# Performance work log

Hardware: AMD Instinct MI355X
Metric: run time of the kernel (lower is better)

Reference implementation:

```python
import jax, jax.numpy as jnp
import numpy as np

B, T, F, H = 4096, 48, 64, 128


def _uniform(key, shape, stdv):
    return jax.random.uniform(key, shape, jnp.float32, -stdv, stdv)


def setup_inputs() -> dict:
    key = jax.random.key(0)
    ks = jax.random.split(key, 24)
    values = jax.random.normal(ks[0], (B, T, F), jnp.float32)
    masks = (jax.random.uniform(ks[1], (B, T, F)) < 0.8).astype(jnp.float32)
    deltas = jax.random.uniform(ks[2], (B, T, F), jnp.float32)
    sH = 1.0 / np.sqrt(H)
    sF = 1.0 / np.sqrt(F)
    inp = {
        "values": values, "masks": masks, "deltas": deltas,
        # TemporalDecay h: W [H, F], b [H] (stdv = 1/sqrt(out=H))
        "Wdh": _uniform(ks[3], (H, F), sH), "bdh": _uniform(ks[4], (H,), sH),
        # TemporalDecay x (diag): W [F, F], b [F]
        "Wdx": _uniform(ks[5], (F, F), sF), "bdx": _uniform(ks[6], (F,), sF),
        # hist_reg: Linear(H -> F)
        "Wh": _uniform(ks[7], (F, H), sH), "bh": _uniform(ks[8], (F,), sH),
        # feat_reg: masked F x F
        "Wf": _uniform(ks[9], (F, F), sF), "bf": _uniform(ks[10], (F,), sF),
        # weight_combine: Linear(2F -> F)
        "Wc": _uniform(ks[11], (F, 2 * F), 1.0 / np.sqrt(2 * F)),
        "bc": _uniform(ks[12], (F,), 1.0 / np.sqrt(2 * F)),
        # LSTMCell(2F -> H): gates in PyTorch order i, f, g, o
        "W_ih": _uniform(ks[13], (4 * H, 2 * F), sH),
        "W_hh": _uniform(ks[14], (4 * H, H), sH),
        "b_ih": _uniform(ks[15], (4 * H,), sH),
        "b_hh": _uniform(ks[16], (4 * H,), sH),
        # out: Linear(H -> 1)
        "Wo": _uniform(ks[17], (1, H), sH), "bo": _uniform(ks[18], (1,), sH),
    }
    return inp


def reference(values, masks, deltas, Wdh, bdh, Wdx, bdx, Wh, bh, Wf, bf,
              Wc, bc, W_ih, W_hh, b_ih, b_hh, Wo, bo):
    impute_weight = 1.0
    b, t, f = values.shape
    h_dim = Wdh.shape[0]
    eye = jnp.eye(f, dtype=values.dtype)
    Wdx_m = Wdx * eye            # diagonal temporal decay
    Wf_m = Wf * (1.0 - eye)

    def step(carry, xt):
        h, c, loss = carry
        x, m, d = xt  # each [B, F]
        gamma_h = jnp.exp(-jax.nn.relu(d @ Wdh.T + bdh))        # [B, H]
        gamma_x = jnp.exp(-jax.nn.relu(d @ Wdx_m.T + bdx))      # [B, F]
        h = h * gamma_h
        x_h = h @ Wh.T + bh
        denom = jnp.sum(m) + 1e-5
        loss = loss + jnp.sum(jnp.abs(x - x_h) * m) / denom
        x_c = m * x + (1.0 - m) * x_h
        z_h = x_c @ Wf_m.T + bf
        loss = loss + jnp.sum(jnp.abs(x - z_h) * m) / denom
        alpha = jnp.concatenate([gamma_x, m], axis=1) @ Wc.T + bc
        c_h = alpha * z_h + (1.0 - alpha) * x_h
        loss = loss + jnp.sum(jnp.abs(x - c_h) * m) / denom
        c_c = m * x + (1.0 - m) * c_h
        inputs = jnp.concatenate([c_c, m], axis=1)  # [B, 2F]
        gates = inputs @ W_ih.T + b_ih + h @ W_hh.T + b_hh
        i_g, f_g, g_g, o_g = jnp.split(gates, 4, axis=1)
        c = jax.nn.sigmoid(f_g) * c + jax.nn.sigmoid(i_g) * jnp.tanh(g_g)
        h = jax.nn.sigmoid(o_g) * jnp.tanh(c)
        return (h, c, loss), c_c

    init = (jnp.zeros((b, h_dim), values.dtype),
            jnp.zeros((b, h_dim), values.dtype),
            jnp.zeros((), values.dtype))
    xs = (jnp.swapaxes(values, 0, 1),
          jnp.swapaxes(masks, 0, 1),
          jnp.swapaxes(deltas, 0, 1))
    (h, c, x_loss), imps = jax.lax.scan(step, init, xs)
    imputations = jnp.swapaxes(imps, 0, 1)  # [B, T, F]
    predictions = h @ Wo.T + bo             # [B, 1]
    return x_loss * impute_weight, imputations, predictions
```

## Files before the change

kernel.cpp:

```cpp
#include <hip/hip_runtime.h>
#include <hip/hip_bf16.h>
#include <math.h>

#define BB 4096
#define TT 48
#define FF 64
#define HH 128
#define ROWS 16
#define NT 512
#define NBLK (BB / ROWS)

typedef __attribute__((ext_vector_type(8))) short short8;
typedef __attribute__((ext_vector_type(4))) float f32x4;

#define MFMA(a, b, c) __builtin_amdgcn_mfma_f32_16x16x32_bf16((a), (b), (c), 0, 0, 0)

__device__ __forceinline__ float sigm(float x) { return 1.f / (1.f + __expf(-x)); }
__device__ __forceinline__ float tanh_f(float x) { return 2.f / (1.f + __expf(-2.f * x)) - 1.f; }

__global__ __launch_bounds__(256) void prep_kernel(
    const float* __restrict__ W_ih, const float* __restrict__ W_hh,
    const float* __restrict__ Wdh,  const float* __restrict__ Wh,
    const float* __restrict__ Wf,   const float* __restrict__ Wc,
    __hip_bfloat16* __restrict__ frags) {
    const int idx = blockIdx.x * 256 + threadIdx.x;
    float v;
    if (idx < 131072) {
        const int jj = idx & 7;
        const int lane = (idx >> 3) & 63;
        const int ks = (idx >> 9) & 7;
        const int tile = idx >> 12;
        const int n = tile * 16 + (lane & 15);
        const int k = ks * 32 + ((lane >> 4) << 3) + jj;
        v = (k < 128) ? W_ih[n * 128 + k] : W_hh[n * 128 + (k - 128)];
    } else {
        const int u = idx - 131072;
        const int jj = u & 7;
        const int lane = (u >> 3) & 63;
        const int lq = lane & 15, q8 = (lane >> 4) << 3;
        if (u < 8192) {
            const int ks = (u >> 9) & 1, nt = u >> 10;
            const int n = nt * 16 + lq, k = ks * 32 + q8 + jj;
            v = Wdh[n * 64 + k];
        } else if (u < 16384) {
            const int uu = u - 8192;
            const int ks = (uu >> 9) & 3, nt = uu >> 11;
            const int n = nt * 16 + lq, k = ks * 32 + q8 + jj;
            v = Wh[n * 128 + k];
        } else if (u < 20480) {
            const int uu = u - 16384;
            const int ks = (uu >> 9) & 1, nt = uu >> 10;
            const int n = nt * 16 + lq, k = ks * 32 + q8 + jj;
            v = (k == n) ? 0.f : Wf[n * 64 + k];
        } else {
            const int uu = u - 20480;
            const int ks = (uu >> 9) & 3, nt = uu >> 11;
            const int n = nt * 16 + lq, k = ks * 32 + q8 + jj;
            v = Wc[n * 128 + k];
        }
    }
    frags[idx] = __float2bfloat16(v);
}

__global__ __launch_bounds__(256) void denom1_kernel(const float* __restrict__ masks,
                                                     float* __restrict__ partials) {
    const int t = blockIdx.x >> 5;
    const int s = blockIdx.x & 31;
    const int tid = threadIdx.x;
    float acc = 0.f;
    #pragma unroll
    for (int k = 0; k < 8; ++k) {
        const int i = k * 256 + tid;
        const int b = s * 128 + (i >> 4);
        const int f = (i & 15) << 2;
        const float4 v = *(const float4*)&masks[((size_t)b * TT + t) * FF + f];
        acc += v.x + v.y + v.z + v.w;
    }
    #pragma unroll
    for (int off = 32; off; off >>= 1) acc += __shfl_down(acc, off, 64);
    __shared__ float red[4];
    if ((tid & 63) == 0) red[tid >> 6] = acc;
    __syncthreads();
    if (tid == 0) partials[blockIdx.x] = red[0] + red[1] + red[2] + red[3];
}

__global__ __launch_bounds__(64) void denom2_kernel(const float* __restrict__ partials,
                                                    float* __restrict__ inv_denom) {
    const int t = threadIdx.x;
    if (t < TT) {
        float s = 0.f;
        #pragma unroll
        for (int i = 0; i < 32; ++i) s += partials[t * 32 + i];
        inv_denom[t] = 1.f / (s + 1e-5f);
    }
}

__global__ __launch_bounds__(NT, 2) void rits_kernel(
    const float* __restrict__ values, const float* __restrict__ masks,
    const float* __restrict__ deltas,
    const float* __restrict__ Wdx, const float* __restrict__ bdx,
    const float* __restrict__ bdh, const float* __restrict__ bh,
    const float* __restrict__ bf,  const float* __restrict__ bc,
    const float* __restrict__ b_ih, const float* __restrict__ b_hh,
    const float* __restrict__ Wo,  const float* __restrict__ bo,
    const __hip_bfloat16* __restrict__ frags,
    const float* __restrict__ inv_denom,
    float* __restrict__ ws_lossblk,
    float* __restrict__ out_imp, float* __restrict__ out_pred)
{
    __shared__ __hip_bfloat16 dbuf[ROWS][72];
    __shared__ __hip_bfloat16 gxbuf[ROWS][72];
    __shared__ __hip_bfloat16 mbuf[ROWS][72];
    __shared__ __hip_bfloat16 xcbuf[ROWS][72];
    __shared__ __hip_bfloat16 ccbuf[ROWS][72];
    __shared__ __hip_bfloat16 hbufB[ROWS][136];
    __shared__ float x_lds[ROWS][65];
    __shared__ float m_lds[ROWS][65];
    __shared__ float redl[8];

    const int tid = threadIdx.x;
    const int bid = blockIdx.x;
    const int b0 = bid * ROWS;
    const int lane = tid & 63;
    const int wv = tid >> 6;
    const int quad = lane >> 4;
    const int lq = lane & 15;
    const int wv3 = wv & 3;

    const float wdx_l = Wdx[lane * (FF + 1)];
    const float bdx_l = bdx[lane];

    const int j_ln = wv * 16 + lq;
    const float bdh_w = bdh[j_ln];
    const float bI = b_ih[j_ln]       + b_hh[j_ln];
    const float bF = b_ih[128 + j_ln] + b_hh[128 + j_ln];
    const float bG = b_ih[256 + j_ln] + b_hh[256 + j_ln];
    const float bO = b_ih[384 + j_ln] + b_hh[384 + j_ln];

    const int f46 = wv3 * 16 + lq;
    const float bh_f = bh[f46];
    const float bf_f = bf[f46];
    const float bc_f = bc[f46];

    const short8* f8 = (const short8*)frags;

    short8 Bgam[2], Bal[4], Bxh[4], Bzh[2];
    #pragma unroll
    for (int ks = 0; ks < 2; ++ks) Bgam[ks] = f8[16384 + ((wv * 2 + ks) << 6) + lane];
    #pragma unroll
    for (int ks = 0; ks < 4; ++ks) Bal[ks] = f8[18944 + ((wv3 * 4 + ks) << 6) + lane];
    #pragma unroll
    for (int ks = 0; ks < 4; ++ks) Bxh[ks] = f8[17408 + ((wv3 * 4 + ks) << 6) + lane];
    #pragma unroll
    for (int ks = 0; ks < 2; ++ks) Bzh[ks] = f8[18432 + ((wv3 * 2 + ks) << 6) + lane];

    const int gbase = (wv << 9) + lane;

    float c_reg[4], h_reg[4];
    #pragma unroll
    for (int r = 0; r < 4; ++r) { c_reg[r] = 0.f; h_reg[r] = 0.f; }
    float loss_acc = 0.f;

    const int base0 = ((b0 + wv) * TT) * FF + lane;
    const int base1 = ((b0 + wv + 8) * TT) * FF + lane;
    const int imp0  = ((b0 + quad * 4) * TT) * FF + f46;

    float xn0 = values[base0], mn0 = masks[base0], dn0 = deltas[base0];
    float xn1 = values[base1], mn1 = masks[base1], dn1 = deltas[base1];
    {
        const int r0 = wv, r1 = wv + 8;
        x_lds[r0][lane] = xn0; m_lds[r0][lane] = mn0;
        dbuf[r0][lane]  = __float2bfloat16(dn0);
        gxbuf[r0][lane] = __float2bfloat16(__expf(-fmaxf(fmaf(dn0, wdx_l, bdx_l), 0.f)));
        mbuf[r0][lane]  = __float2bfloat16(mn0);
        x_lds[r1][lane] = xn1; m_lds[r1][lane] = mn1;
        dbuf[r1][lane]  = __float2bfloat16(dn1);
        gxbuf[r1][lane] = __float2bfloat16(__expf(-fmaxf(fmaf(dn1, wdx_l, bdx_l), 0.f)));
        mbuf[r1][lane]  = __float2bfloat16(mn1);
    }
    __syncthreads();

    for (int t = 0; t < TT; ++t) {
        const float invd = inv_denom[t];

        {
            const int tn = (t < TT - 1) ? t + 1 : t;
            const int o0 = base0 + tn * FF, o1 = base1 + tn * FF;
            xn0 = values[o0]; mn0 = masks[o0]; dn0 = deltas[o0];
            xn1 = values[o1]; mn1 = masks[o1]; dn1 = deltas[o1];
        }
        float al_r[4];
        {
            f32x4 ga = {0.f, 0.f, 0.f, 0.f};
            #pragma unroll
            for (int ks = 0; ks < 2; ++ks) {
                const short8 a = *(const short8*)&dbuf[lq][ks * 32 + quad * 8];
                ga = MFMA(a, Bgam[ks], ga);
            }
            if (wv < 4) {
                f32x4 aa = {0.f, 0.f, 0.f, 0.f};
                #pragma unroll
                for (int ks = 0; ks < 2; ++ks) {
                    const short8 a = *(const short8*)&gxbuf[lq][ks * 32 + quad * 8];
                    aa = MFMA(a, Bal[ks], aa);
                }
                #pragma unroll
                for (int ks = 2; ks < 4; ++ks) {
                    const short8 a = *(const short8*)&mbuf[lq][(ks - 2) * 32 + quad * 8];
                    aa = MFMA(a, Bal[ks], aa);
                }
                #pragma unroll
                for (int r = 0; r < 4; ++r) al_r[r] = aa[r] + bc_f;
            }
            #pragma unroll
            for (int r = 0; r < 4; ++r) {
                const float gh = __expf(-fmaxf(ga[r] + bdh_w, 0.f));
                hbufB[quad * 4 + r][j_ln] = __float2bfloat16(h_reg[r] * gh);
            }
        }
        __syncthreads();

        f32x4 gacc0 = {0.f,0.f,0.f,0.f}, gacc1 = {0.f,0.f,0.f,0.f};
        f32x4 gacc2 = {0.f,0.f,0.f,0.f}, gacc3 = {0.f,0.f,0.f,0.f};
        #pragma unroll
        for (int ks = 4; ks < 8; ++ks) {
            const short8 a = *(const short8*)&hbufB[lq][(ks - 4) * 32 + quad * 8];
            gacc0 = MFMA(a, f8[gbase + 0     + (ks << 6)], gacc0);
            gacc1 = MFMA(a, f8[gbase + 4096  + (ks << 6)], gacc1);
            gacc2 = MFMA(a, f8[gbase + 8192  + (ks << 6)], gacc2);
            gacc3 = MFMA(a, f8[gbase + 12288 + (ks << 6)], gacc3);
        }
        float xv_r[4], mv_r[4], xh_r[4];
        float stepsum = 0.f;
        if (wv < 4) {
            f32x4 acc = {0.f, 0.f, 0.f, 0.f};
            #pragma unroll
            for (int ks = 0; ks < 4; ++ks) {
                const short8 a = *(const short8*)&hbufB[lq][ks * 32 + quad * 8];
                acc = MFMA(a, Bxh[ks], acc);
            }
            #pragma unroll
            for (int r = 0; r < 4; ++r) {
                const int row = quad * 4 + r;
                const float xh = acc[r] + bh_f;
                xh_r[r] = xh;
                const float xv = x_lds[row][f46], mv = m_lds[row][f46];
                xv_r[r] = xv; mv_r[r] = mv;
                stepsum += mv * fabsf(xv - xh);
                xcbuf[row][f46] = __float2bfloat16(fmaf(mv, xv, (1.f - mv) * xh));
            }
        }
        __syncthreads();

        #pragma unroll
        for (int ks = 2; ks < 4; ++ks) {
            const short8 a = *(const short8*)&mbuf[lq][(ks - 2) * 32 + quad * 8];
            gacc0 = MFMA(a, f8[gbase + 0     + (ks << 6)], gacc0);
            gacc1 = MFMA(a, f8[gbase + 4096  + (ks << 6)], gacc1);
            gacc2 = MFMA(a, f8[gbase + 8192  + (ks << 6)], gacc2);
            gacc3 = MFMA(a, f8[gbase + 12288 + (ks << 6)], gacc3);
        }
        if (wv < 4) {
            f32x4 acc5 = {0.f, 0.f, 0.f, 0.f};
            #pragma unroll
            for (int ks = 0; ks < 2; ++ks) {
                const short8 a = *(const short8*)&xcbuf[lq][ks * 32 + quad * 8];
                acc5 = MFMA(a, Bzh[ks], acc5);
            }
            #pragma unroll
            for (int r = 0; r < 4; ++r) {
                const int row = quad * 4 + r;
                const float zh = acc5[r] + bf_f;
                stepsum += mv_r[r] * fabsf(xv_r[r] - zh);
                const float alpha = al_r[r];
                const float ch = fmaf(alpha, zh, (1.f - alpha) * xh_r[r]);
                stepsum += mv_r[r] * fabsf(xv_r[r] - ch);
                const float cc = fmaf(mv_r[r], xv_r[r], (1.f - mv_r[r]) * ch);
                ccbuf[row][f46] = __float2bfloat16(cc);
                out_imp[imp0 + r * (TT * FF) + t * FF] = cc;
            }
        }
        loss_acc = fmaf(stepsum, invd, loss_acc);
        __syncthreads();

        #pragma unroll
        for (int ks = 0; ks < 2; ++ks) {
            const short8 a = *(const short8*)&ccbuf[lq][ks * 32 + quad * 8];
            gacc0 = MFMA(a, f8[gbase + 0     + (ks << 6)], gacc0);
            gacc1 = MFMA(a, f8[gbase + 4096  + (ks << 6)], gacc1);
            gacc2 = MFMA(a, f8[gbase + 8192  + (ks << 6)], gacc2);
            gacc3 = MFMA(a, f8[gbase + 12288 + (ks << 6)], gacc3);
        }
        {
            const int r0 = wv, r1 = wv + 8;
            x_lds[r0][lane] = xn0; m_lds[r0][lane] = mn0;
            dbuf[r0][lane]  = __float2bfloat16(dn0);
            gxbuf[r0][lane] = __float2bfloat16(__expf(-fmaxf(fmaf(dn0, wdx_l, bdx_l), 0.f)));
            mbuf[r0][lane]  = __float2bfloat16(mn0);
            x_lds[r1][lane] = xn1; m_lds[r1][lane] = mn1;
            dbuf[r1][lane]  = __float2bfloat16(dn1);
            gxbuf[r1][lane] = __float2bfloat16(__expf(-fmaxf(fmaf(dn1, wdx_l, bdx_l), 0.f)));
            mbuf[r1][lane]  = __float2bfloat16(mn1);
        }
        #pragma unroll
        for (int r = 0; r < 4; ++r) {
            const float ig = sigm(gacc0[r] + bI);
            const float fg = sigm(gacc1[r] + bF);
            const float gg = tanh_f(gacc2[r] + bG);
            const float og = sigm(gacc3[r] + bO);
            c_reg[r] = fmaf(fg, c_reg[r], ig * gg);
            h_reg[r] = og * tanh_f(c_reg[r]);
        }
        __syncthreads();
    }

    #pragma unroll
    for (int r = 0; r < 4; ++r)
        hbufB[quad * 4 + r][j_ln] = __float2bfloat16(h_reg[r]);
    __syncthreads();
    {
        const int r = tid >> 5, l = tid & 31;
        float s = 0.f;
        #pragma unroll
        for (int k = l; k < HH; k += 32) s += __bfloat162float(hbufB[r][k]) * Wo[k];
        #pragma unroll
        for (int off = 16; off; off >>= 1) s += __shfl_down(s, off, 32);
        if (l == 0) out_pred[b0 + r] = s + bo[0];
    }
    #pragma unroll
    for (int off = 32; off; off >>= 1) loss_acc += __shfl_down(loss_acc, off, 64);
    if (lane == 0) redl[wv] = loss_acc;
    __syncthreads();
    if (tid == 0) {
        float s = 0.f;
        #pragma unroll
        for (int w = 0; w < 8; ++w) s += redl[w];
        ws_lossblk[bid] = s;
    }
}

__global__ __launch_bounds__(256) void final_kernel(const float* __restrict__ ws_lossblk,
                                                    float* __restrict__ out_loss) {
    const int tid = threadIdx.x;
    float s = ws_lossblk[tid];
    #pragma unroll
    for (int off = 32; off; off >>= 1) s += __shfl_down(s, off, 64);
    __shared__ float red[4];
    if ((tid & 63) == 0) red[tid >> 6] = s;
    __syncthreads();
    if (tid == 0) out_loss[0] = red[0] + red[1] + red[2] + red[3];
}

extern "C" void kernel_launch(void* const* d_in, const int* in_sizes, int n_in,
                              void* d_out, int out_size, void* d_ws, size_t ws_size,
                              hipStream_t stream) {
    const float* values = (const float*)d_in[0];
    const float* masks  = (const float*)d_in[1];
    const float* deltas = (const float*)d_in[2];
    const float* Wdh  = (const float*)d_in[3];
    const float* bdh  = (const float*)d_in[4];
    const float* Wdx  = (const float*)d_in[5];
    const float* bdx  = (const float*)d_in[6];
    const float* Wh   = (const float*)d_in[7];
    const float* bh   = (const float*)d_in[8];
    const float* Wf   = (const float*)d_in[9];
    const float* bf   = (const float*)d_in[10];
    const float* Wc   = (const float*)d_in[11];
    const float* bc   = (const float*)d_in[12];
    const float* W_ih = (const float*)d_in[13];
    const float* W_hh = (const float*)d_in[14];
    const float* b_ih = (const float*)d_in[15];
    const float* b_hh = (const float*)d_in[16];
    const float* Wo   = (const float*)d_in[17];
    const float* bo   = (const float*)d_in[18];

    __hip_bfloat16* frags = (__hip_bfloat16*)d_ws;
    float* inv_denom  = (float*)((char*)d_ws + 320 * 1024);
    float* partials   = inv_denom + 64;
    float* ws_lossblk = partials + 2048;

    float* out_loss = (float*)d_out;
    float* out_imp  = out_loss + 1;
    float* out_pred = out_imp + (size_t)BB * TT * FF;

    prep_kernel<<<624, 256, 0, stream>>>(W_ih, W_hh, Wdh, Wh, Wf, Wc, frags);
    denom1_kernel<<<TT * 32, 256, 0, stream>>>(masks, partials);
    denom2_kernel<<<1, 64, 0, stream>>>(partials, inv_denom);
    rits_kernel<<<NBLK, NT, 0, stream>>>(
        values, masks, deltas, Wdx, bdx, bdh, bh, bf, bc,
        b_ih, b_hh, Wo, bo, frags, inv_denom, ws_lossblk, out_imp, out_pred);
    final_kernel<<<1, 256, 0, stream>>>(ws_lossblk, out_loss);
}
```

Baseline: 362.8 us.

## Stage LSTM gate weights in registers and LDS instead of per-step global loads

The input-side LSTM weight fragments (for c_c and mask) are now held in registers for the whole kernel, and the recurrent W_hh fragments are copied once into a 128 KB LDS array. Each time step reads them from registers or LDS instead of from global/L2 memory. The mask-gate MFMAs are moved to the start of the step, and the h-gate MFMAs are split across two phases. This adds many VGPRs and a large LDS footprint, which may reduce occupancy below the two-blocks-per-CU launch bound.

```diff
diff --git a/kernel.cpp b/kernel.cpp
--- a/kernel.cpp
+++ b/kernel.cpp
@@ -108,6 +108,7 @@
     float* __restrict__ ws_lossblk,
     float* __restrict__ out_imp, float* __restrict__ out_pred)
 {
+    __shared__ short8 whh_frag[8192];
     __shared__ __hip_bfloat16 dbuf[ROWS][72];
     __shared__ __hip_bfloat16 gxbuf[ROWS][72];
     __shared__ __hip_bfloat16 mbuf[ROWS][72];
@@ -154,7 +155,21 @@
     #pragma unroll
     for (int ks = 0; ks < 2; ++ks) Bzh[ks] = f8[18432 + ((wv3 * 2 + ks) << 6) + lane];
 
-    const int gbase = (wv << 9) + lane;
+    short8 Bcc[4][2], Bm[4][2];
+    #pragma unroll
+    for (int g = 0; g < 4; ++g) {
+        #pragma unroll
+        for (int kk = 0; kk < 2; ++kk) {
+            Bcc[g][kk] = f8[(((g * 8 + wv) * 8 + kk)     << 6) + lane];
+            Bm[g][kk]  = f8[(((g * 8 + wv) * 8 + 2 + kk) << 6) + lane];
+        }
+    }
+    for (int i = tid; i < 8192; i += NT) {
+        const int slot = i >> 6, ln = i & 63;
+        const int g = slot >> 5, rem = slot & 31, j = rem >> 2, kk = rem & 3;
+        whh_frag[i] = f8[(((g * 8 + j) * 8 + 4 + kk) << 6) + ln];
+    }
+    const int wbase = (wv << 8) + lane;
 
     float c_reg[4], h_reg[4];
     #pragma unroll
@@ -188,6 +203,16 @@
             const int o0 = base0 + tn * FF, o1 = base1 + tn * FF;
             xn0 = values[o0]; mn0 = masks[o0]; dn0 = deltas[o0];
             xn1 = values[o1]; mn1 = masks[o1]; dn1 = deltas[o1];
+        }
+        f32x4 gacc0 = {0.f,0.f,0.f,0.f}, gacc1 = {0.f,0.f,0.f,0.f};
+        f32x4 gacc2 = {0.f,0.f,0.f,0.f}, gacc3 = {0.f,0.f,0.f,0.f};
+        #pragma unroll
+        for (int kk = 0; kk < 2; ++kk) {
+            const short8 a = *(const short8*)&mbuf[lq][kk * 32 + quad * 8];
+            gacc0 = MFMA(a, Bm[0][kk], gacc0);
+            gacc1 = MFMA(a, Bm[1][kk], gacc1);
+            gacc2 = MFMA(a, Bm[2][kk], gacc2);
+            gacc3 = MFMA(a, Bm[3][kk], gacc3);
         }
         float al_r[4];
         {
@@ -220,15 +245,13 @@
         }
         __syncthreads();
 
-        f32x4 gacc0 = {0.f,0.f,0.f,0.f}, gacc1 = {0.f,0.f,0.f,0.f};
-        f32x4 gacc2 = {0.f,0.f,0.f,0.f}, gacc3 = {0.f,0.f,0.f,0.f};
-        #pragma unroll
-        for (int ks = 4; ks < 8; ++ks) {
-            const short8 a = *(const short8*)&hbufB[lq][(ks - 4) * 32 + quad * 8];
-            gacc0 = MFMA(a, f8[gbase + 0     + (ks << 6)], gacc0);
-            gacc1 = MFMA(a, f8[gbase + 4096  + (ks << 6)], gacc1);
-            gacc2 = MFMA(a, f8[gbase + 8192  + (ks << 6)], gacc2);
-            gacc3 = MFMA(a, f8[gbase + 12288 + (ks << 6)], gacc3);
+        #pragma unroll
+        for (int kk = 0; kk < 2; ++kk) {
+            const short8 a = *(const short8*)&hbufB[lq][kk * 32 + quad * 8];
+            gacc0 = MFMA(a, whh_frag[wbase + 0    + kk * 64], gacc0);
+            gacc1 = MFMA(a, whh_frag[wbase + 2048 + kk * 64], gacc1);
+            gacc2 = MFMA(a, whh_frag[wbase + 4096 + kk * 64], gacc2);
+            gacc3 = MFMA(a, whh_frag[wbase + 6144 + kk * 64], gacc3);
         }
         float xv_r[4], mv_r[4], xh_r[4];
         float stepsum = 0.f;
@@ -253,12 +276,12 @@
         __syncthreads();
 
         #pragma unroll
-        for (int ks = 2; ks < 4; ++ks) {
-            const short8 a = *(const short8*)&mbuf[lq][(ks - 2) * 32 + quad * 8];
-            gacc0 = MFMA(a, f8[gbase + 0     + (ks << 6)], gacc0);
-            gacc1 = MFMA(a, f8[gbase + 4096  + (ks << 6)], gacc1);
-            gacc2 = MFMA(a, f8[gbase + 8192  + (ks << 6)], gacc2);
-            gacc3 = MFMA(a, f8[gbase + 12288 + (ks << 6)], gacc3);
+        for (int kk = 2; kk < 4; ++kk) {
+            const short8 a = *(const short8*)&hbufB[lq][kk * 32 + quad * 8];
+            gacc0 = MFMA(a, whh_frag[wbase + 0    + kk * 64], gacc0);
+            gacc1 = MFMA(a, whh_frag[wbase + 2048 + kk * 64], gacc1);
+            gacc2 = MFMA(a, whh_frag[wbase + 4096 + kk * 64], gacc2);
+            gacc3 = MFMA(a, whh_frag[wbase + 6144 + kk * 64], gacc3);
         }
         if (wv < 4) {
             f32x4 acc5 = {0.f, 0.f, 0.f, 0.f};
@@ -284,12 +307,12 @@
         __syncthreads();
 
         #pragma unroll
-        for (int ks = 0; ks < 2; ++ks) {
-            const short8 a = *(const short8*)&ccbuf[lq][ks * 32 + quad * 8];
-            gacc0 = MFMA(a, f8[gbase + 0     + (ks << 6)], gacc0);
-            gacc1 = MFMA(a, f8[gbase + 4096  + (ks << 6)], gacc1);
-            gacc2 = MFMA(a, f8[gbase + 8192  + (ks << 6)], gacc2);
-            gacc3 = MFMA(a, f8[gbase + 12288 + (ks << 6)], gacc3);
+        for (int kk = 0; kk < 2; ++kk) {
+            const short8 a = *(const short8*)&ccbuf[lq][kk * 32 + quad * 8];
+            gacc0 = MFMA(a, Bcc[0][kk], gacc0);
+            gacc1 = MFMA(a, Bcc[1][kk], gacc1);
+            gacc2 = MFMA(a, Bcc[2][kk], gacc2);
+            gacc3 = MFMA(a, Bcc[3][kk], gacc3);
         }
         {
             const int r0 = wv, r1 = wv + 8;
```

New measurement: 318.4 us. 1.14x faster.
